# Kernel optimization log

Hardware: AMD Instinct MI355X
Metric: run time of the kernel (lower is better)

The kernel has to match this reference:

```python
import jax, jax.numpy as jnp
import numpy as np

N, E, T = 25000, 400000, 4          # nodes, edges, edge types (one-hot width)
NODE_DIM, EDGE_DIM = 128, 64        # raw feature dims
NO, EO, OUT = 32, 64, 128           # node_ft_out_dim, edge_ft_out_dim, out_dim
D = NO + EO + NO                    # z_node_lv_dim = 128


def segment_softmax(scores, seg, num_segments):
    """Numerically stable softmax over variable-sized segments (1D scores)."""
    m = jax.ops.segment_max(scores, seg, num_segments=num_segments)
    ex = jnp.exp(scores - m[seg])
    den = jax.ops.segment_sum(ex, seg, num_segments=num_segments)
    return ex / den[seg]


def setup_inputs() -> dict:
    key = jax.random.key(0)
    ks = jax.random.split(key, 11)
    node_features = jax.random.normal(ks[0], (N, NODE_DIM), dtype=jnp.float32)
    edge_features = jax.random.normal(ks[1], (E, EDGE_DIM), dtype=jnp.float32)
    src = jax.random.randint(ks[2], (E,), 0, N, dtype=jnp.int32)
    dst = jax.random.randint(ks[3], (E,), 0, N, dtype=jnp.int32)
    edge_type_idx = jax.random.randint(ks[4], (E,), 0, T, dtype=jnp.int32)
    # learned params (torch Linear stored transposed: we use [in, out])
    W_n = jax.random.normal(ks[5], (NODE_DIM, NO), dtype=jnp.float32) / np.sqrt(NODE_DIM)
    W_e = jax.random.normal(ks[6], (EDGE_DIM, EO), dtype=jnp.float32) / np.sqrt(EDGE_DIM)
    w_eattn = jax.random.normal(ks[7], (EO + NO,), dtype=jnp.float32) / np.sqrt(EO + NO)
    w_attn = jax.random.normal(ks[8], (D,), dtype=jnp.float32) / np.sqrt(D)
    w_sem = jax.random.normal(ks[9], (D,), dtype=jnp.float32) / np.sqrt(D)
    W_fc2 = jax.random.normal(ks[10], (D, OUT), dtype=jnp.float32) / np.sqrt(D)
    return {
        "node_features": node_features, "edge_features": edge_features,
        "src": src, "dst": dst, "edge_type_idx": edge_type_idx,
        "W_n": W_n, "W_e": W_e, "w_eattn": w_eattn, "w_attn": w_attn,
        "w_sem": w_sem, "W_fc2": W_fc2,
    }


def reference(node_features, edge_features, src, dst, edge_type_idx,
              W_n, W_e, w_eattn, w_attn, w_sem, W_fc2):
    n = node_features.shape[0]
    # --- WeightedAggEdge: project, then softmax edge weights grouped by SRC ---
    z = node_features @ W_n                      # [N, NO]
    e_ft = edge_features @ W_e                   # [E, EO]
    z_src = z[src]                               # [E, NO]
    s1 = jax.nn.leaky_relu(jnp.concatenate([e_ft, z_src], axis=1) @ w_eattn)  # [E]
    gamma = segment_softmax(s1, src, n)          # softmax over edges sharing src
    e_w = gamma[:, None] * e_ft                  # [E, EO]
    # --- BaseGAT_Modified: edge attention + softmax over DST mailboxes ---
    z_dst = z[dst]                               # [E, NO]
    # message z == z2 == [src z, e_weighted, dst z]
    msg = jnp.concatenate([z_src, e_w, z_dst], axis=1)   # [E, D]
    s2 = jax.nn.leaky_relu(msg @ w_attn)         # [E]
    alpha = segment_softmax(s2, dst, n)          # softmax over incoming edges
    weighted = alpha[:, None] * msg              # [E, D]
    # type-grouped scatter-sum: out[dst, t] += onehot(type)[t] * weighted
    seg = dst * T + edge_type_idx                # fused (node, type) segment id
    h = jax.ops.segment_sum(weighted, seg, num_segments=n * T).reshape(n, T, D)
    # --- SemLevelGAT: semantic attention over edge types ---
    zphi = h.sum(axis=0)                         # [T, D]
    beta = jax.nn.softmax(jax.nn.leaky_relu(zphi @ w_sem))   # [T]
    Z = jnp.einsum('t,ntd->nd', beta, h) @ W_fc2             # [N, OUT]
    return Z, e_w
```

## Files before the change

### kernel.cpp

```cpp
#include <hip/hip_runtime.h>

#define NN 25000
#define NE 400000
#define TT 4
#define NO 32
#define EO 64
#define DD 128
#define OUTD 128
#define ZGRID 2048

#define OFF_Z      0
#define OFF_ASRC   800000
#define OFF_BSRC   825000
#define OFF_BDST   850000
#define OFF_C1     875000
#define OFF_C2     1275000
#define OFF_S1X    1675000
#define OFF_GAMMA  2075000
#define OFF_S2X    2475000
#define OFF_DEN1   2875000
#define OFF_DEN2   2900000
#define OFF_ZPHI   2925000
#define OFF_BETA   2925512
#define OFF_CSRC   2926000
#define OFF_CDST   3026000
#define OFF_DEG    3126000
#define OFF_OFFS   3151000
#define OFF_CURSOR 3176004
#define OFF_EIDX   3201004
#define OFF_HBETA  3601004
#define WS_FLOATS  6801004

__device__ __forceinline__ float lrelu(float x) { return x > 0.f ? x : 0.01f * x; }

__global__ __launch_bounds__(256) void k_node(const float* __restrict__ nf,
    const float* __restrict__ W_n, const float* __restrict__ w_eattn,
    const float* __restrict__ w_attn, float* __restrict__ z,
    float* __restrict__ a_src, float* __restrict__ b_src, float* __restrict__ b_dst)
{
    __shared__ float Wl[128 * 32];
    __shared__ float nl[8 * 128];
    int tid = threadIdx.x;
    for (int i = tid; i < 128 * 32 / 4; i += 256)
        ((float4*)Wl)[i] = ((const float4*)W_n)[i];
    int nb = blockIdx.x * 8;
    ((float4*)nl)[tid] = ((const float4*)(nf + (size_t)nb * 128))[tid];
    __syncthreads();
    int node = tid >> 5;
    int col = tid & 31;
    float acc = 0.f;
    #pragma unroll 8
    for (int k = 0; k < 128; ++k)
        acc += nl[node * 128 + k] * Wl[k * 32 + col];
    int n = nb + node;
    z[(size_t)n * 32 + col] = acc;
    float va = acc * w_eattn[64 + col];
    float vb = acc * w_attn[col];
    float vc = acc * w_attn[96 + col];
    #pragma unroll
    for (int m = 16; m >= 1; m >>= 1) {
        va += __shfl_xor(va, m);
        vb += __shfl_xor(vb, m);
        vc += __shfl_xor(vc, m);
    }
    if (col == 0) { a_src[n] = va; b_src[n] = vb; b_dst[n] = vc; }
}

__global__ __launch_bounds__(256) void k_edge(const float* __restrict__ ef,
    const float* __restrict__ W_e, const float* __restrict__ w_eattn,
    const float* __restrict__ w_attn, float* __restrict__ eft_out,
    float* __restrict__ c1, float* __restrict__ c2)
{
    __shared__ float Wl[32 * 64];
    __shared__ float el[64 * 36];
    int tid = threadIdx.x;
    size_t eb = (size_t)blockIdx.x * 64;
    int cgrp = tid & 15, egrp = tid >> 4;
    int c0 = cgrp * 4;
    int e0 = egrp * 4;
    float acc[4][4];
    #pragma unroll
    for (int i = 0; i < 4; ++i)
        #pragma unroll
        for (int j = 0; j < 4; ++j) acc[i][j] = 0.f;
    for (int h = 0; h < 2; ++h) {
        __syncthreads();
        for (int i = tid; i < 512; i += 256)
            ((float4*)Wl)[i] = ((const float4*)(W_e + h * 32 * 64))[i];
        for (int i = tid; i < 512; i += 256) {
            int e = i >> 3, q = i & 7;
            float4 v = *(const float4*)&ef[(eb + e) * 64 + h * 32 + q * 4];
            *(float4*)&el[e * 36 + q * 4] = v;
        }
        __syncthreads();
        #pragma unroll
        for (int k0 = 0; k0 < 32; k0 += 4) {
            float4 a[4], w[4];
            #pragma unroll
            for (int e = 0; e < 4; ++e) a[e] = *(const float4*)&el[(e0 + e) * 36 + k0];
            #pragma unroll
            for (int j = 0; j < 4; ++j) w[j] = *(const float4*)&Wl[(k0 + j) * 64 + c0];
            #pragma unroll
            for (int e = 0; e < 4; ++e) {
                acc[e][0] += a[e].x * w[0].x + a[e].y * w[1].x + a[e].z * w[2].x + a[e].w * w[3].x;
                acc[e][1] += a[e].x * w[0].y + a[e].y * w[1].y + a[e].z * w[2].y + a[e].w * w[3].y;
                acc[e][2] += a[e].x * w[0].z + a[e].y * w[1].z + a[e].z * w[2].z + a[e].w * w[3].z;
                acc[e][3] += a[e].x * w[0].w + a[e].y * w[1].w + a[e].z * w[2].w + a[e].w * w[3].w;
            }
        }
    }
    float4 we1 = *(const float4*)&w_eattn[c0];
    float4 we2 = *(const float4*)&w_attn[32 + c0];
    #pragma unroll
    for (int e = 0; e < 4; ++e) {
        float4 o; o.x = acc[e][0]; o.y = acc[e][1]; o.z = acc[e][2]; o.w = acc[e][3];
        *(float4*)&eft_out[(eb + e0 + e) * 64 + c0] = o;
        float p1 = o.x * we1.x + o.y * we1.y + o.z * we1.z + o.w * we1.w;
        float p2 = o.x * we2.x + o.y * we2.y + o.z * we2.z + o.w * we2.w;
        #pragma unroll
        for (int m = 8; m >= 1; m >>= 1) {
            p1 += __shfl_xor(p1, m);
            p2 += __shfl_xor(p2, m);
        }
        if (cgrp == 0) { c1[eb + e0 + e] = p1; c2[eb + e0 + e] = p2; }
    }
}

__global__ void k_s1ex(const float* __restrict__ c1, const float* __restrict__ a_src,
                       const int* __restrict__ src, const int* __restrict__ dst,
                       float* __restrict__ s1x, float* __restrict__ den1, int* __restrict__ deg)
{
    int e = blockIdx.x * 256 + threadIdx.x;
    if (e >= NE) return;
    int s = src[e];
    float ex = expf(lrelu(c1[e] + a_src[s]));
    s1x[e] = ex;
    atomicAdd(&den1[s], ex);
    atomicAdd(&deg[dst[e]], 1);
}

__global__ __launch_bounds__(1024) void k_scan(const int* __restrict__ deg,
    int* __restrict__ offs, int* __restrict__ cursor)
{
    __shared__ int wsum[16];
    __shared__ int carry_s;
    int tid = threadIdx.x;
    int lane = tid & 63, wid = tid >> 6;
    if (tid == 0) carry_s = 0;
    __syncthreads();
    for (int base = 0; base < NN; base += 1024) {
        int idx = base + tid;
        int v = (idx < NN) ? deg[idx] : 0;
        int x = v;
        #pragma unroll
        for (int off = 1; off < 64; off <<= 1) {
            int t = __shfl_up(x, off);
            if (lane >= off) x += t;
        }
        if (lane == 63) wsum[wid] = x;
        __syncthreads();
        if (wid == 0) {
            int s = (lane < 16) ? wsum[lane] : 0;
            #pragma unroll
            for (int off = 1; off < 16; off <<= 1) {
                int t = __shfl_up(s, off);
                if (lane >= off) s += t;
            }
            if (lane < 16) wsum[lane] = s;
        }
        __syncthreads();
        int wbase = (wid > 0) ? wsum[wid - 1] : 0;
        int incl = x + wbase;
        int carry = carry_s;
        if (idx < NN) {
            int excl = carry + incl - v;
            offs[idx] = excl;
            cursor[idx] = excl;
        }
        __syncthreads();
        if (tid == 1023) carry_s = carry + incl;
        __syncthreads();
    }
    if (tid == 0) offs[NN] = carry_s;
}

__global__ void k_g2ex(const int* __restrict__ src, const int* __restrict__ dst,
    const float* __restrict__ s1x, const float* __restrict__ den1,
    const float* __restrict__ c2, const float* __restrict__ b_src, const float* __restrict__ b_dst,
    float* __restrict__ gamma, float* __restrict__ s2x, float* __restrict__ den2,
    int* __restrict__ cursor, int* __restrict__ eidx)
{
    int e = blockIdx.x * 256 + threadIdx.x;
    if (e >= NE) return;
    int s = src[e], t = dst[e];
    float g = s1x[e] / den1[s];
    gamma[e] = g;
    float ex = expf(lrelu(b_src[s] + g * c2[e] + b_dst[t]));
    s2x[e] = ex;
    atomicAdd(&den2[t], ex);
    int pos = atomicAdd(&cursor[t], 1);
    eidx[pos] = e;
}

__global__ __launch_bounds__(256) void k_zphi_stream(const int* __restrict__ src,
    const int* __restrict__ dst, const int* __restrict__ ety,
    const float* __restrict__ s2x, const float* __restrict__ den2,
    const float* __restrict__ gamma, float* __restrict__ ew, float* __restrict__ alpha,
    float* __restrict__ csrc, float* __restrict__ cdst, float* __restrict__ zpart)
{
    __shared__ float zl[256];
    int tid = threadIdx.x;
    zl[tid] = 0.f;
    __syncthreads();
    int sub = tid & 15, grp = tid >> 4;
    int d0 = sub * 4;
    float4 a0 = make_float4(0, 0, 0, 0), a1 = a0, a2 = a0, a3 = a0;
    int G = ZGRID * 16;
    for (int e = blockIdx.x * 16 + grp; e < NE; e += 2 * G) {
        int e2 = e + G;
        bool h2 = e2 < NE;
        int dnA = dst[e];   float sA = s2x[e];  float gA = gamma[e];  int tA = ety[e];
        int dnB = 0; float sB = 0.f, gB = 0.f; int tB = 0;
        if (h2) { dnB = dst[e2]; sB = s2x[e2]; gB = gamma[e2]; tB = ety[e2]; }
        float alA = sA / den2[dnA];
        float alB = h2 ? sB / den2[dnB] : 0.f;
        if (sub == 0) { alpha[e] = alA; if (h2) alpha[e2] = alB; }
        if (sub == 1) {
            atomicAdd(&csrc[src[e] * 4 + tA], alA);
            if (h2) atomicAdd(&csrc[src[e2] * 4 + tB], alB);
        }
        if (sub == 2) {
            atomicAdd(&cdst[dnA * 4 + tA], alA);
            if (h2) atomicAdd(&cdst[dnB * 4 + tB], alB);
        }
        float4 rA = *(const float4*)&ew[(size_t)e * 64 + d0];
        float4 mA; mA.x = gA * rA.x; mA.y = gA * rA.y; mA.z = gA * rA.z; mA.w = gA * rA.w;
        *(float4*)&ew[(size_t)e * 64 + d0] = mA;
        float4 mB = make_float4(0, 0, 0, 0);
        if (h2) {
            float4 rB = *(const float4*)&ew[(size_t)e2 * 64 + d0];
            mB.x = gB * rB.x; mB.y = gB * rB.y; mB.z = gB * rB.z; mB.w = gB * rB.w;
            *(float4*)&ew[(size_t)e2 * 64 + d0] = mB;
        }
        float wA0 = (tA == 0) ? alA : 0.f, wA1 = (tA == 1) ? alA : 0.f;
        float wA2 = (tA == 2) ? alA : 0.f, wA3 = (tA == 3) ? alA : 0.f;
        float wB0 = (h2 && tB == 0) ? alB : 0.f, wB1 = (h2 && tB == 1) ? alB : 0.f;
        float wB2 = (h2 && tB == 2) ? alB : 0.f, wB3 = (h2 && tB == 3) ? alB : 0.f;
        a0.x += wA0 * mA.x + wB0 * mB.x; a0.y += wA0 * mA.y + wB0 * mB.y;
        a0.z += wA0 * mA.z + wB0 * mB.z; a0.w += wA0 * mA.w + wB0 * mB.w;
        a1.x += wA1 * mA.x + wB1 * mB.x; a1.y += wA1 * mA.y + wB1 * mB.y;
        a1.z += wA1 * mA.z + wB1 * mB.z; a1.w += wA1 * mA.w + wB1 * mB.w;
        a2.x += wA2 * mA.x + wB2 * mB.x; a2.y += wA2 * mA.y + wB2 * mB.y;
        a2.z += wA2 * mA.z + wB2 * mB.z; a2.w += wA2 * mA.w + wB2 * mB.w;
        a3.x += wA3 * mA.x + wB3 * mB.x; a3.y += wA3 * mA.y + wB3 * mB.y;
        a3.z += wA3 * mA.z + wB3 * mB.z; a3.w += wA3 * mA.w + wB3 * mB.w;
    }
    #pragma unroll
    for (int m = 16; m <= 32; m <<= 1) {
        a0.x += __shfl_xor(a0.x, m); a0.y += __shfl_xor(a0.y, m);
        a0.z += __shfl_xor(a0.z, m); a0.w += __shfl_xor(a0.w, m);
        a1.x += __shfl_xor(a1.x, m); a1.y += __shfl_xor(a1.y, m);
        a1.z += __shfl_xor(a1.z, m); a1.w += __shfl_xor(a1.w, m);
        a2.x += __shfl_xor(a2.x, m); a2.y += __shfl_xor(a2.y, m);
        a2.z += __shfl_xor(a2.z, m); a2.w += __shfl_xor(a2.w, m);
        a3.x += __shfl_xor(a3.x, m); a3.y += __shfl_xor(a3.y, m);
        a3.z += __shfl_xor(a3.z, m); a3.w += __shfl_xor(a3.w, m);
    }
    if ((tid & 63) < 16) {
        atomicAdd(&zl[0 * 64 + d0 + 0], a0.x); atomicAdd(&zl[0 * 64 + d0 + 1], a0.y);
        atomicAdd(&zl[0 * 64 + d0 + 2], a0.z); atomicAdd(&zl[0 * 64 + d0 + 3], a0.w);
        atomicAdd(&zl[1 * 64 + d0 + 0], a1.x); atomicAdd(&zl[1 * 64 + d0 + 1], a1.y);
        atomicAdd(&zl[1 * 64 + d0 + 2], a1.z); atomicAdd(&zl[1 * 64 + d0 + 3], a1.w);
        atomicAdd(&zl[2 * 64 + d0 + 0], a2.x); atomicAdd(&zl[2 * 64 + d0 + 1], a2.y);
        atomicAdd(&zl[2 * 64 + d0 + 2], a2.z); atomicAdd(&zl[2 * 64 + d0 + 3], a2.w);
        atomicAdd(&zl[3 * 64 + d0 + 0], a3.x); atomicAdd(&zl[3 * 64 + d0 + 1], a3.y);
        atomicAdd(&zl[3 * 64 + d0 + 2], a3.z); atomicAdd(&zl[3 * 64 + d0 + 3], a3.w);
    }
    __syncthreads();
    zpart[(size_t)blockIdx.x * 256 + tid] = zl[tid];
}

__global__ __launch_bounds__(256) void k_zphi_red(const float* __restrict__ zpart,
    float* __restrict__ zphi)
{
    int tid = threadIdx.x;
    float s = 0.f;
    int r0 = blockIdx.x * 32;
    for (int r = r0; r < r0 + 32; ++r)
        s += zpart[(size_t)r * 256 + tid];
    atomicAdd(&zphi[(tid >> 6) * 128 + 32 + (tid & 63)], s);
}

__global__ __launch_bounds__(256) void k_zphi_nodes(const float* __restrict__ z,
    const float* __restrict__ csrc, const float* __restrict__ cdst, float* __restrict__ zphi)
{
    __shared__ float zl[256];
    int tid = threadIdx.x;
    zl[tid] = 0.f;
    __syncthreads();
    int d = tid & 31, ng = tid >> 5;
    float s0 = 0, s1 = 0, s2 = 0, s3 = 0, t0 = 0, t1 = 0, t2 = 0, t3 = 0;
    for (int n = blockIdx.x * 8 + ng; n < NN; n += gridDim.x * 8) {
        float zv = z[(size_t)n * 32 + d];
        float4 cs = *(const float4*)&csrc[n * 4];
        float4 cd = *(const float4*)&cdst[n * 4];
        s0 += cs.x * zv; s1 += cs.y * zv; s2 += cs.z * zv; s3 += cs.w * zv;
        t0 += cd.x * zv; t1 += cd.y * zv; t2 += cd.z * zv; t3 += cd.w * zv;
    }
    s0 += __shfl_xor(s0, 32); s1 += __shfl_xor(s1, 32);
    s2 += __shfl_xor(s2, 32); s3 += __shfl_xor(s3, 32);
    t0 += __shfl_xor(t0, 32); t1 += __shfl_xor(t1, 32);
    t2 += __shfl_xor(t2, 32); t3 += __shfl_xor(t3, 32);
    if ((tid & 63) < 32) {
        atomicAdd(&zl[0 * 32 + d], s0); atomicAdd(&zl[1 * 32 + d], s1);
        atomicAdd(&zl[2 * 32 + d], s2); atomicAdd(&zl[3 * 32 + d], s3);
        atomicAdd(&zl[128 + 0 * 32 + d], t0); atomicAdd(&zl[128 + 1 * 32 + d], t1);
        atomicAdd(&zl[128 + 2 * 32 + d], t2); atomicAdd(&zl[128 + 3 * 32 + d], t3);
    }
    __syncthreads();
    if (tid < 128) atomicAdd(&zphi[(tid >> 5) * 128 + (tid & 31)], zl[tid]);
    else atomicAdd(&zphi[((tid - 128) >> 5) * 128 + 96 + (tid & 31)], zl[tid]);
}

__global__ __launch_bounds__(128) void k_beta(const float* __restrict__ zphi,
    const float* __restrict__ w_sem, float* __restrict__ beta)
{
    int tid = threadIdx.x;
    float w = w_sem[tid];
    float p0 = zphi[tid] * w, p1 = zphi[128 + tid] * w;
    float p2 = zphi[256 + tid] * w, p3 = zphi[384 + tid] * w;
    #pragma unroll
    for (int m = 32; m >= 1; m >>= 1) {
        p0 += __shfl_xor(p0, m); p1 += __shfl_xor(p1, m);
        p2 += __shfl_xor(p2, m); p3 += __shfl_xor(p3, m);
    }
    __shared__ float s[2][4];
    if ((tid & 63) == 0) {
        int w_ = tid >> 6;
        s[w_][0] = p0; s[w_][1] = p1; s[w_][2] = p2; s[w_][3] = p3;
    }
    __syncthreads();
    if (tid == 0) {
        float d0 = lrelu(s[0][0] + s[1][0]);
        float d1 = lrelu(s[0][1] + s[1][1]);
        float d2 = lrelu(s[0][2] + s[1][2]);
        float d3 = lrelu(s[0][3] + s[1][3]);
        float mx = fmaxf(fmaxf(d0, d1), fmaxf(d2, d3));
        float e0 = expf(d0 - mx), e1 = expf(d1 - mx), e2 = expf(d2 - mx), e3 = expf(d3 - mx);
        float inv = 1.f / (e0 + e1 + e2 + e3);
        beta[0] = e0 * inv; beta[1] = e1 * inv; beta[2] = e2 * inv; beta[3] = e3 * inv;
    }
}

__global__ void k_walpha(const float* __restrict__ alpha, const int* __restrict__ ety,
                         const float* __restrict__ beta, float* __restrict__ w)
{
    int e = blockIdx.x * 256 + threadIdx.x;
    if (e >= NE) return;
    w[e] = alpha[e] * beta[ety[e]];
}

__global__ __launch_bounds__(256) void k_scatter(const int* __restrict__ offs,
    const int* __restrict__ eidx, const int* __restrict__ src,
    const float* __restrict__ w, const float* __restrict__ z,
    const float* __restrict__ ew, float* __restrict__ hbeta)
{
    int tid = threadIdx.x;
    int lane = tid & 31;
    int grp = tid >> 5;
    int n = blockIdx.x * 8 + grp;
    if (n >= NN) return;
    int d0 = lane * 4;
    int beg = offs[n], end = offs[n + 1];
    float4 acc = make_float4(0, 0, 0, 0);
    float sumw = 0.f;
    int i = beg;
    for (; i + 2 <= end; i += 2) {
        int ea = eidx[i], eb = eidx[i + 1];
        float wa = w[ea], wb = w[eb];
        int sa = src[ea], sb = src[eb];
        sumw += wa + wb;
        if (lane < 24) {
            const float* pa = (lane < 8) ? &z[(size_t)sa * 32 + d0]
                                         : &ew[(size_t)ea * 64 + (d0 - 32)];
            const float* pb = (lane < 8) ? &z[(size_t)sb * 32 + d0]
                                         : &ew[(size_t)eb * 64 + (d0 - 32)];
            float4 ma = *(const float4*)pa;
            float4 mb = *(const float4*)pb;
            acc.x += wa * ma.x + wb * mb.x; acc.y += wa * ma.y + wb * mb.y;
            acc.z += wa * ma.z + wb * mb.z; acc.w += wa * ma.w + wb * mb.w;
        }
    }
    if (i < end) {
        int ea = eidx[i];
        float wa = w[ea];
        int sa = src[ea];
        sumw += wa;
        if (lane < 24) {
            const float* pa = (lane < 8) ? &z[(size_t)sa * 32 + d0]
                                         : &ew[(size_t)ea * 64 + (d0 - 32)];
            float4 ma = *(const float4*)pa;
            acc.x += wa * ma.x; acc.y += wa * ma.y; acc.z += wa * ma.z; acc.w += wa * ma.w;
        }
    }
    if (lane >= 24) {
        float4 zd = *(const float4*)&z[(size_t)n * 32 + (d0 - 96)];
        acc.x = sumw * zd.x; acc.y = sumw * zd.y; acc.z = sumw * zd.z; acc.w = sumw * zd.w;
    }
    *(float4*)&hbeta[(size_t)n * 128 + d0] = acc;
}

__global__ __launch_bounds__(256) void k_fc(const float* __restrict__ hb,
    const float* __restrict__ W, float* __restrict__ Z)
{
    __shared__ float hl[32 * 132];
    __shared__ float Wl[128 * 64];
    int tid = threadIdx.x;
    int nb = blockIdx.x * 32;
    for (int i = tid; i < 1024; i += 256) {
        int row = i >> 5, kc = (i & 31) * 4;
        float4 v = make_float4(0.f, 0.f, 0.f, 0.f);
        if (nb + row < NN) v = *(const float4*)&hb[(size_t)(nb + row) * 128 + kc];
        *(float4*)&hl[row * 132 + kc] = v;
    }
    for (int half = 0; half < 2; ++half) {
        __syncthreads();
        for (int i = tid; i < 2048; i += 256) {
            int k = i >> 4, c = (i & 15) * 4;
            *(float4*)&Wl[k * 64 + c] = *(const float4*)&W[(size_t)k * 128 + half * 64 + c];
        }
        __syncthreads();
        int node = tid >> 3;
        int c0 = (tid & 7) * 8;
        float acc[8] = {0, 0, 0, 0, 0, 0, 0, 0};
        #pragma unroll 4
        for (int k = 0; k < 128; ++k) {
            float a = hl[node * 132 + k];
            const float* wr = &Wl[k * 64 + c0];
            #pragma unroll
            for (int j = 0; j < 8; ++j) acc[j] += a * wr[j];
        }
        int n = nb + node;
        if (n < NN) {
            float4 o1, o2;
            o1.x = acc[0]; o1.y = acc[1]; o1.z = acc[2]; o1.w = acc[3];
            o2.x = acc[4]; o2.y = acc[5]; o2.z = acc[6]; o2.w = acc[7];
            *(float4*)&Z[(size_t)n * 128 + half * 64 + c0] = o1;
            *(float4*)&Z[(size_t)n * 128 + half * 64 + c0 + 4] = o2;
        }
    }
}

extern "C" void kernel_launch(void* const* d_in, const int* in_sizes, int n_in,
                              void* d_out, int out_size, void* d_ws, size_t ws_size,
                              hipStream_t stream)
{
    const float* nf     = (const float*)d_in[0];
    const float* ef     = (const float*)d_in[1];
    const int*   src    = (const int*)d_in[2];
    const int*   dst    = (const int*)d_in[3];
    const int*   ety    = (const int*)d_in[4];
    const float* W_n    = (const float*)d_in[5];
    const float* W_e    = (const float*)d_in[6];
    const float* w_eattn= (const float*)d_in[7];
    const float* w_attn = (const float*)d_in[8];
    const float* w_sem  = (const float*)d_in[9];
    const float* W_fc2  = (const float*)d_in[10];

    float* out = (float*)d_out;
    float* Z   = out;
    float* ew  = out + (size_t)NN * OUTD;

    float* ws    = (float*)d_ws;
    float* z     = ws + OFF_Z;
    float* a_src = ws + OFF_ASRC;
    float* b_src = ws + OFF_BSRC;
    float* b_dst = ws + OFF_BDST;
    float* c1    = ws + OFF_C1;
    float* c2    = ws + OFF_C2;
    float* s1x   = ws + OFF_S1X;
    float* gamma = ws + OFF_GAMMA;
    float* s2x   = ws + OFF_S2X;
    float* alpha = ws + OFF_S1X;
    float* wgt   = ws + OFF_GAMMA;
    float* zpart = ws + OFF_C1;
    float* den1  = ws + OFF_DEN1;
    float* den2  = ws + OFF_DEN2;
    float* zphi  = ws + OFF_ZPHI;
    float* beta  = ws + OFF_BETA;
    float* csrc  = ws + OFF_CSRC;
    float* cdst  = ws + OFF_CDST;
    int* deg     = (int*)(ws + OFF_DEG);
    int* offs    = (int*)(ws + OFF_OFFS);
    int* cursor  = (int*)(ws + OFF_CURSOR);
    int* eidx    = (int*)(ws + OFF_EIDX);
    float* hbeta = ws + OFF_HBETA;

    hipMemsetAsync(ws + OFF_DEN1, 0, (size_t)(OFF_OFFS - OFF_DEN1) * 4, stream);

    k_node<<<NN / 8, 256, 0, stream>>>(nf, W_n, w_eattn, w_attn, z, a_src, b_src, b_dst);
    k_edge<<<NE / 64, 256, 0, stream>>>(ef, W_e, w_eattn, w_attn, ew, c1, c2);
    int gE = (NE + 255) / 256;
    k_s1ex<<<gE, 256, 0, stream>>>(c1, a_src, src, dst, s1x, den1, deg);
    k_scan<<<1, 1024, 0, stream>>>(deg, offs, cursor);
    k_g2ex<<<gE, 256, 0, stream>>>(src, dst, s1x, den1, c2, b_src, b_dst, gamma, s2x, den2, cursor, eidx);
    k_zphi_stream<<<ZGRID, 256, 0, stream>>>(src, dst, ety, s2x, den2, gamma, ew, alpha, csrc, cdst, zpart);
    k_zphi_red<<<ZGRID / 32, 256, 0, stream>>>(zpart, zphi);
    k_zphi_nodes<<<128, 256, 0, stream>>>(z, csrc, cdst, zphi);
    k_beta<<<1, 128, 0, stream>>>(zphi, w_sem, beta);
    k_walpha<<<gE, 256, 0, stream>>>(alpha, ety, beta, wgt);
    k_scatter<<<(NN + 7) / 8, 256, 0, stream>>>(offs, eidx, src, wgt, z, ew, hbeta);
    k_fc<<<(NN + 31) / 32, 256, 0, stream>>>(hbeta, W_fc2, Z);
}
```

Measured before the change: 360.1 us.

## Fold edge projection into attention vectors and fuse the e_ft recompute with the zphi reduction

The edge attention scores c1 and c2 are now computed directly from the raw edge features, using two 64-wide vectors u1 and u2. These are precomputed as W_e times the relevant attention weight slices, so the scores no longer wait on the full edge projection. The edge GEMM is moved later into a persistent kernel that recomputes e_ft, scales it by gamma, writes e_w once, and accumulates per-type partial sums into shared memory with atomics. This removes the write-then-read-modify-write round trip of the [E,64] e_ft buffer, at the cost of reading edge_features twice, adding a separate alpha kernel, and adding per-element shared-memory atomics.

```diff
diff --git a/kernel.cpp b/kernel.cpp
--- a/kernel.cpp
+++ b/kernel.cpp
@@ -13,23 +13,25 @@
 #define OFF_ASRC   800000
 #define OFF_BSRC   825000
 #define OFF_BDST   850000
-#define OFF_C1     875000
-#define OFF_C2     1275000
-#define OFF_S1X    1675000
-#define OFF_GAMMA  2075000
-#define OFF_S2X    2475000
-#define OFF_DEN1   2875000
-#define OFF_DEN2   2900000
-#define OFF_ZPHI   2925000
-#define OFF_BETA   2925512
-#define OFF_CSRC   2926000
-#define OFF_CDST   3026000
-#define OFF_DEG    3126000
-#define OFF_OFFS   3151000
-#define OFF_CURSOR 3176004
-#define OFF_EIDX   3201004
-#define OFF_HBETA  3601004
-#define WS_FLOATS  6801004
+#define OFF_ZPART  875000
+#define OFF_C2     1400000
+#define OFF_S1X    1800000
+#define OFF_GAMMA  2200000
+#define OFF_S2X    2600000
+#define OFF_DEN1   3000000
+#define OFF_DEN2   3025000
+#define OFF_ZPHI   3050000
+#define OFF_BETA   3050512
+#define OFF_CSRC   3051000
+#define OFF_CDST   3151000
+#define OFF_DEG    3251000
+#define OFF_OFFS   3276000
+#define OFF_CURSOR 3301004
+#define OFF_EIDX   3326004
+#define OFF_HBETA  3726008
+#define OFF_U1     6926008
+#define OFF_U2     6926072
+#define WS_FLOATS  6926136
 
 __device__ __forceinline__ float lrelu(float x) { return x > 0.f ? x : 0.01f * x; }
 
@@ -66,77 +68,46 @@
     if (col == 0) { a_src[n] = va; b_src[n] = vb; b_dst[n] = vc; }
 }
 
-__global__ __launch_bounds__(256) void k_edge(const float* __restrict__ ef,
-    const float* __restrict__ W_e, const float* __restrict__ w_eattn,
-    const float* __restrict__ w_attn, float* __restrict__ eft_out,
-    float* __restrict__ c1, float* __restrict__ c2)
-{
-    __shared__ float Wl[32 * 64];
-    __shared__ float el[64 * 36];
-    int tid = threadIdx.x;
-    size_t eb = (size_t)blockIdx.x * 64;
-    int cgrp = tid & 15, egrp = tid >> 4;
-    int c0 = cgrp * 4;
-    int e0 = egrp * 4;
-    float acc[4][4];
-    #pragma unroll
-    for (int i = 0; i < 4; ++i)
-        #pragma unroll
-        for (int j = 0; j < 4; ++j) acc[i][j] = 0.f;
-    for (int h = 0; h < 2; ++h) {
-        __syncthreads();
-        for (int i = tid; i < 512; i += 256)
-            ((float4*)Wl)[i] = ((const float4*)(W_e + h * 32 * 64))[i];
-        for (int i = tid; i < 512; i += 256) {
-            int e = i >> 3, q = i & 7;
-            float4 v = *(const float4*)&ef[(eb + e) * 64 + h * 32 + q * 4];
-            *(float4*)&el[e * 36 + q * 4] = v;
-        }
-        __syncthreads();
-        #pragma unroll
-        for (int k0 = 0; k0 < 32; k0 += 4) {
-            float4 a[4], w[4];
-            #pragma unroll
-            for (int e = 0; e < 4; ++e) a[e] = *(const float4*)&el[(e0 + e) * 36 + k0];
-            #pragma unroll
-            for (int j = 0; j < 4; ++j) w[j] = *(const float4*)&Wl[(k0 + j) * 64 + c0];
-            #pragma unroll
-            for (int e = 0; e < 4; ++e) {
-                acc[e][0] += a[e].x * w[0].x + a[e].y * w[1].x + a[e].z * w[2].x + a[e].w * w[3].x;
-                acc[e][1] += a[e].x * w[0].y + a[e].y * w[1].y + a[e].z * w[2].y + a[e].w * w[3].y;
-                acc[e][2] += a[e].x * w[0].z + a[e].y * w[1].z + a[e].z * w[2].z + a[e].w * w[3].z;
-                acc[e][3] += a[e].x * w[0].w + a[e].y * w[1].w + a[e].z * w[2].w + a[e].w * w[3].w;
-            }
-        }
-    }
-    float4 we1 = *(const float4*)&w_eattn[c0];
-    float4 we2 = *(const float4*)&w_attn[32 + c0];
-    #pragma unroll
-    for (int e = 0; e < 4; ++e) {
-        float4 o; o.x = acc[e][0]; o.y = acc[e][1]; o.z = acc[e][2]; o.w = acc[e][3];
-        *(float4*)&eft_out[(eb + e0 + e) * 64 + c0] = o;
-        float p1 = o.x * we1.x + o.y * we1.y + o.z * we1.z + o.w * we1.w;
-        float p2 = o.x * we2.x + o.y * we2.y + o.z * we2.z + o.w * we2.w;
+__global__ void k_vec(const float* __restrict__ W_e, const float* __restrict__ w_eattn,
+                      const float* __restrict__ w_attn, float* __restrict__ u1, float* __restrict__ u2)
+{
+    int i = threadIdx.x;
+    float s1 = 0.f, s2 = 0.f;
+    for (int o = 0; o < 64; ++o) {
+        float w = W_e[i * 64 + o];
+        s1 += w * w_eattn[o];
+        s2 += w * w_attn[32 + o];
+    }
+    u1[i] = s1; u2[i] = s2;
+}
+
+__global__ __launch_bounds__(256) void k_c12s1(const float* __restrict__ ef,
+    const float* __restrict__ u1, const float* __restrict__ u2,
+    const float* __restrict__ a_src, const int* __restrict__ src, const int* __restrict__ dst,
+    float* __restrict__ c2, float* __restrict__ s1x, float* __restrict__ den1, int* __restrict__ deg)
+{
+    int lane = threadIdx.x & 15, grp = threadIdx.x >> 4;
+    float4 v1 = *(const float4*)&u1[lane * 4];
+    float4 v2 = *(const float4*)&u2[lane * 4];
+    int estep = gridDim.x * 16;
+    for (int e = blockIdx.x * 16 + grp; e < NE; e += estep) {
+        float4 x = *(const float4*)&ef[(size_t)e * 64 + lane * 4];
+        float d1 = x.x * v1.x + x.y * v1.y + x.z * v1.z + x.w * v1.w;
+        float d2 = x.x * v2.x + x.y * v2.y + x.z * v2.z + x.w * v2.w;
         #pragma unroll
         for (int m = 8; m >= 1; m >>= 1) {
-            p1 += __shfl_xor(p1, m);
-            p2 += __shfl_xor(p2, m);
-        }
-        if (cgrp == 0) { c1[eb + e0 + e] = p1; c2[eb + e0 + e] = p2; }
-    }
-}
-
-__global__ void k_s1ex(const float* __restrict__ c1, const float* __restrict__ a_src,
-                       const int* __restrict__ src, const int* __restrict__ dst,
-                       float* __restrict__ s1x, float* __restrict__ den1, int* __restrict__ deg)
-{
-    int e = blockIdx.x * 256 + threadIdx.x;
-    if (e >= NE) return;
-    int s = src[e];
-    float ex = expf(lrelu(c1[e] + a_src[s]));
-    s1x[e] = ex;
-    atomicAdd(&den1[s], ex);
-    atomicAdd(&deg[dst[e]], 1);
+            d1 += __shfl_xor(d1, m);
+            d2 += __shfl_xor(d2, m);
+        }
+        if (lane == 0) {
+            int s = src[e];
+            float ex = expf(lrelu(d1 + a_src[s]));
+            s1x[e] = ex;
+            c2[e] = d2;
+            atomicAdd(&den1[s], ex);
+            atomicAdd(&deg[dst[e]], 1);
+        }
+    }
 }
 
 __global__ __launch_bounds__(1024) void k_scan(const int* __restrict__ deg,
@@ -202,79 +173,82 @@
     eidx[pos] = e;
 }
 
-__global__ __launch_bounds__(256) void k_zphi_stream(const int* __restrict__ src,
-    const int* __restrict__ dst, const int* __restrict__ ety,
-    const float* __restrict__ s2x, const float* __restrict__ den2,
-    const float* __restrict__ gamma, float* __restrict__ ew, float* __restrict__ alpha,
-    float* __restrict__ csrc, float* __restrict__ cdst, float* __restrict__ zpart)
-{
+__global__ void k_alpha(const int* __restrict__ src, const int* __restrict__ dst,
+    const int* __restrict__ ety, const float* __restrict__ s2x, const float* __restrict__ den2,
+    float* __restrict__ alpha, float* __restrict__ csrc, float* __restrict__ cdst)
+{
+    int e = blockIdx.x * 256 + threadIdx.x;
+    if (e >= NE) return;
+    int t = dst[e];
+    int ty = ety[e];
+    float al = s2x[e] / den2[t];
+    alpha[e] = al;
+    atomicAdd(&csrc[src[e] * 4 + ty], al);
+    atomicAdd(&cdst[t * 4 + ty], al);
+}
+
+__global__ __launch_bounds__(256) void k_edge_fused(const float* __restrict__ ef,
+    const float* __restrict__ W_e, const float* __restrict__ gamma,
+    const float* __restrict__ alpha, const int* __restrict__ ety,
+    float* __restrict__ ew, float* __restrict__ zpart)
+{
+    __shared__ float Wl[32 * 64];
+    __shared__ float el[64 * 36];
     __shared__ float zl[256];
     int tid = threadIdx.x;
     zl[tid] = 0.f;
-    __syncthreads();
-    int sub = tid & 15, grp = tid >> 4;
-    int d0 = sub * 4;
-    float4 a0 = make_float4(0, 0, 0, 0), a1 = a0, a2 = a0, a3 = a0;
-    int G = ZGRID * 16;
-    for (int e = blockIdx.x * 16 + grp; e < NE; e += 2 * G) {
-        int e2 = e + G;
-        bool h2 = e2 < NE;
-        int dnA = dst[e];   float sA = s2x[e];  float gA = gamma[e];  int tA = ety[e];
-        int dnB = 0; float sB = 0.f, gB = 0.f; int tB = 0;
-        if (h2) { dnB = dst[e2]; sB = s2x[e2]; gB = gamma[e2]; tB = ety[e2]; }
-        float alA = sA / den2[dnA];
-        float alB = h2 ? sB / den2[dnB] : 0.f;
-        if (sub == 0) { alpha[e] = alA; if (h2) alpha[e2] = alB; }
-        if (sub == 1) {
-            atomicAdd(&csrc[src[e] * 4 + tA], alA);
-            if (h2) atomicAdd(&csrc[src[e2] * 4 + tB], alB);
-        }
-        if (sub == 2) {
-            atomicAdd(&cdst[dnA * 4 + tA], alA);
-            if (h2) atomicAdd(&cdst[dnB * 4 + tB], alB);
-        }
-        float4 rA = *(const float4*)&ew[(size_t)e * 64 + d0];
-        float4 mA; mA.x = gA * rA.x; mA.y = gA * rA.y; mA.z = gA * rA.z; mA.w = gA * rA.w;
-        *(float4*)&ew[(size_t)e * 64 + d0] = mA;
-        float4 mB = make_float4(0, 0, 0, 0);
-        if (h2) {
-            float4 rB = *(const float4*)&ew[(size_t)e2 * 64 + d0];
-            mB.x = gB * rB.x; mB.y = gB * rB.y; mB.z = gB * rB.z; mB.w = gB * rB.w;
-            *(float4*)&ew[(size_t)e2 * 64 + d0] = mB;
-        }
-        float wA0 = (tA == 0) ? alA : 0.f, wA1 = (tA == 1) ? alA : 0.f;
-        float wA2 = (tA == 2) ? alA : 0.f, wA3 = (tA == 3) ? alA : 0.f;
-        float wB0 = (h2 && tB == 0) ? alB : 0.f, wB1 = (h2 && tB == 1) ? alB : 0.f;
-        float wB2 = (h2 && tB == 2) ? alB : 0.f, wB3 = (h2 && tB == 3) ? alB : 0.f;
-        a0.x += wA0 * mA.x + wB0 * mB.x; a0.y += wA0 * mA.y + wB0 * mB.y;
-        a0.z += wA0 * mA.z + wB0 * mB.z; a0.w += wA0 * mA.w + wB0 * mB.w;
-        a1.x += wA1 * mA.x + wB1 * mB.x; a1.y += wA1 * mA.y + wB1 * mB.y;
-        a1.z += wA1 * mA.z + wB1 * mB.z; a1.w += wA1 * mA.w + wB1 * mB.w;
-        a2.x += wA2 * mA.x + wB2 * mB.x; a2.y += wA2 * mA.y + wB2 * mB.y;
-        a2.z += wA2 * mA.z + wB2 * mB.z; a2.w += wA2 * mA.w + wB2 * mB.w;
-        a3.x += wA3 * mA.x + wB3 * mB.x; a3.y += wA3 * mA.y + wB3 * mB.y;
-        a3.z += wA3 * mA.z + wB3 * mB.z; a3.w += wA3 * mA.w + wB3 * mB.w;
-    }
-    #pragma unroll
-    for (int m = 16; m <= 32; m <<= 1) {
-        a0.x += __shfl_xor(a0.x, m); a0.y += __shfl_xor(a0.y, m);
-        a0.z += __shfl_xor(a0.z, m); a0.w += __shfl_xor(a0.w, m);
-        a1.x += __shfl_xor(a1.x, m); a1.y += __shfl_xor(a1.y, m);
-        a1.z += __shfl_xor(a1.z, m); a1.w += __shfl_xor(a1.w, m);
-        a2.x += __shfl_xor(a2.x, m); a2.y += __shfl_xor(a2.y, m);
-        a2.z += __shfl_xor(a2.z, m); a2.w += __shfl_xor(a2.w, m);
-        a3.x += __shfl_xor(a3.x, m); a3.y += __shfl_xor(a3.y, m);
-        a3.z += __shfl_xor(a3.z, m); a3.w += __shfl_xor(a3.w, m);
-    }
-    if ((tid & 63) < 16) {
-        atomicAdd(&zl[0 * 64 + d0 + 0], a0.x); atomicAdd(&zl[0 * 64 + d0 + 1], a0.y);
-        atomicAdd(&zl[0 * 64 + d0 + 2], a0.z); atomicAdd(&zl[0 * 64 + d0 + 3], a0.w);
-        atomicAdd(&zl[1 * 64 + d0 + 0], a1.x); atomicAdd(&zl[1 * 64 + d0 + 1], a1.y);
-        atomicAdd(&zl[1 * 64 + d0 + 2], a1.z); atomicAdd(&zl[1 * 64 + d0 + 3], a1.w);
-        atomicAdd(&zl[2 * 64 + d0 + 0], a2.x); atomicAdd(&zl[2 * 64 + d0 + 1], a2.y);
-        atomicAdd(&zl[2 * 64 + d0 + 2], a2.z); atomicAdd(&zl[2 * 64 + d0 + 3], a2.w);
-        atomicAdd(&zl[3 * 64 + d0 + 0], a3.x); atomicAdd(&zl[3 * 64 + d0 + 1], a3.y);
-        atomicAdd(&zl[3 * 64 + d0 + 2], a3.z); atomicAdd(&zl[3 * 64 + d0 + 3], a3.w);
+    int cgrp = tid & 15, egrp = tid >> 4;
+    int c0 = cgrp * 4;
+    int e0 = egrp * 4;
+    for (int tile = blockIdx.x; tile < NE / 64; tile += gridDim.x) {
+        size_t eb = (size_t)tile * 64;
+        float acc[4][4];
+        #pragma unroll
+        for (int i = 0; i < 4; ++i)
+            #pragma unroll
+            for (int j = 0; j < 4; ++j) acc[i][j] = 0.f;
+        for (int h = 0; h < 2; ++h) {
+            __syncthreads();
+            for (int i = tid; i < 512; i += 256)
+                ((float4*)Wl)[i] = ((const float4*)(W_e + h * 32 * 64))[i];
+            for (int i = tid; i < 512; i += 256) {
+                int e = i >> 3, q = i & 7;
+                float4 v = *(const float4*)&ef[(eb + e) * 64 + h * 32 + q * 4];
+                *(float4*)&el[e * 36 + q * 4] = v;
+            }
+            __syncthreads();
+            #pragma unroll
+            for (int k0 = 0; k0 < 32; k0 += 4) {
+                float4 a[4], w[4];
+                #pragma unroll
+                for (int e = 0; e < 4; ++e) a[e] = *(const float4*)&el[(e0 + e) * 36 + k0];
+                #pragma unroll
+                for (int j = 0; j < 4; ++j) w[j] = *(const float4*)&Wl[(k0 + j) * 64 + c0];
+                #pragma unroll
+                for (int e = 0; e < 4; ++e) {
+                    acc[e][0] += a[e].x * w[0].x + a[e].y * w[1].x + a[e].z * w[2].x + a[e].w * w[3].x;
+                    acc[e][1] += a[e].x * w[0].y + a[e].y * w[1].y + a[e].z * w[2].y + a[e].w * w[3].y;
+                    acc[e][2] += a[e].x * w[0].z + a[e].y * w[1].z + a[e].z * w[2].z + a[e].w * w[3].z;
+                    acc[e][3] += a[e].x * w[0].w + a[e].y * w[1].w + a[e].z * w[2].w + a[e].w * w[3].w;
+                }
+            }
+        }
+        #pragma unroll
+        for (int e = 0; e < 4; ++e) {
+            size_t eg = eb + e0 + e;
+            float g = gamma[eg];
+            float al = alpha[eg];
+            int t = ety[eg];
+            float4 o;
+            o.x = acc[e][0] * g; o.y = acc[e][1] * g;
+            o.z = acc[e][2] * g; o.w = acc[e][3] * g;
+            *(float4*)&ew[eg * 64 + c0] = o;
+            float* zr = &zl[t * 64 + c0];
+            atomicAdd(zr + 0, al * o.x);
+            atomicAdd(zr + 1, al * o.y);
+            atomicAdd(zr + 2, al * o.z);
+            atomicAdd(zr + 3, al * o.w);
+        }
     }
     __syncthreads();
     zpart[(size_t)blockIdx.x * 256 + tid] = zl[tid];
@@ -476,14 +450,13 @@
     float* a_src = ws + OFF_ASRC;
     float* b_src = ws + OFF_BSRC;
     float* b_dst = ws + OFF_BDST;
-    float* c1    = ws + OFF_C1;
+    float* zpart = ws + OFF_ZPART;
     float* c2    = ws + OFF_C2;
     float* s1x   = ws + OFF_S1X;
     float* gamma = ws + OFF_GAMMA;
     float* s2x   = ws + OFF_S2X;
     float* alpha = ws + OFF_S1X;
     float* wgt   = ws + OFF_GAMMA;
-    float* zpart = ws + OFF_C1;
     float* den1  = ws + OFF_DEN1;
     float* den2  = ws + OFF_DEN2;
     float* zphi  = ws + OFF_ZPHI;
@@ -495,16 +468,19 @@
     int* cursor  = (int*)(ws + OFF_CURSOR);
     int* eidx    = (int*)(ws + OFF_EIDX);
     float* hbeta = ws + OFF_HBETA;
+    float* u1    = ws + OFF_U1;
+    float* u2    = ws + OFF_U2;
 
     hipMemsetAsync(ws + OFF_DEN1, 0, (size_t)(OFF_OFFS - OFF_DEN1) * 4, stream);
 
     k_node<<<NN / 8, 256, 0, stream>>>(nf, W_n, w_eattn, w_attn, z, a_src, b_src, b_dst);
-    k_edge<<<NE / 64, 256, 0, stream>>>(ef, W_e, w_eattn, w_attn, ew, c1, c2);
+    k_vec<<<1, 64, 0, stream>>>(W_e, w_eattn, w_attn, u1, u2);
+    k_c12s1<<<4096, 256, 0, stream>>>(ef, u1, u2, a_src, src, dst, c2, s1x, den1, deg);
+    k_scan<<<1, 1024, 0, stream>>>(deg, offs, cursor);
     int gE = (NE + 255) / 256;
-    k_s1ex<<<gE, 256, 0, stream>>>(c1, a_src, src, dst, s1x, den1, deg);
-    k_scan<<<1, 1024, 0, stream>>>(deg, offs, cursor);
     k_g2ex<<<gE, 256, 0, stream>>>(src, dst, s1x, den1, c2, b_src, b_dst, gamma, s2x, den2, cursor, eidx);
-    k_zphi_stream<<<ZGRID, 256, 0, stream>>>(src, dst, ety, s2x, den2, gamma, ew, alpha, csrc, cdst, zpart);
+    k_alpha<<<gE, 256, 0, stream>>>(src, dst, ety, s2x, den2, alpha, csrc, cdst);
+    k_edge_fused<<<ZGRID, 256, 0, stream>>>(ef, W_e, gamma, alpha, ety, ew, zpart);
     k_zphi_red<<<ZGRID / 32, 256, 0, stream>>>(zpart, zphi);
     k_zphi_nodes<<<128, 256, 0, stream>>>(z, csrc, cdst, zphi);
     k_beta<<<1, 128, 0, stream>>>(zphi, w_sem, beta);
```

After: 475.6 us. 32.1% more time.
